# Kernel tuning notes

Hardware: AMD Instinct MI355X
Metric: run time of the kernel (lower is better)

## Reference

```python
import jax, jax.numpy as jnp
import numpy as np

B, DIM, KEY_DIM, NH, AR, RES, KS = 32, 512, 16, 8, 4, 64, 5
D = AR * KEY_DIM          # 64, per-head value dim
C4 = DIM // 4             # 128, q/k channel dim
CHUNK = DIM // NH         # 64, per-head input chunk
SCALE = KEY_DIM ** -0.5


def setup_inputs() -> dict:
    key = jax.random.key(0)
    ks = jax.random.split(key, 8)
    def rn(k, shape, fan):
        return jax.random.normal(k, shape, jnp.float32) * (fan ** -0.5)
    x = jax.random.normal(ks[0], (B, DIM, RES, RES), jnp.float32)
    qk_w = rn(ks[1], (DIM // 2, DIM), DIM)            # fused 1x1 conv+BN weight
    qk_b = jnp.zeros((DIM // 2,), jnp.float32)
    dws_w = rn(ks[2], (C4, 1, KS, KS), KS * KS)        # depthwise conv weight
    dws_b = jnp.zeros((C4,), jnp.float32)
    vs_w = rn(ks[3], (NH, D, CHUNK), CHUNK)            # per-head 1x1 conv weights
    vs_b = jnp.zeros((NH, D), jnp.float32)
    proj_w = rn(ks[4], (DIM, D * NH), D * NH)
    proj_b = jnp.zeros((DIM,), jnp.float32)
    bias_h = jax.random.normal(ks[5], (1, RES), jnp.float32) * 0.02
    bias_w = jax.random.normal(ks[6], (1, RES), jnp.float32) * 0.02
    # offset id for (p1, p2) is exactly |p1 - p2| given enumeration order
    idx = jnp.abs(jnp.arange(RES)[:, None] - jnp.arange(RES)[None, :]).astype(jnp.int32)
    return dict(x=x, qk_w=qk_w, qk_b=qk_b, dws_w=dws_w, dws_b=dws_b,
                vs_w=vs_w, vs_b=vs_b, proj_w=proj_w, proj_b=proj_b,
                bias_h=bias_h, bias_w=bias_w, idx_h=idx, idx_w=idx)


def reference(x, qk_w, qk_b, dws_w, dws_b, vs_w, vs_b, proj_w, proj_b,
              bias_h, bias_w, idx_h, idx_w):
    ab_h = bias_h[0][idx_h]                               # [N, N]
    ab_w = bias_w[0][idx_w]                               # [N, N]
    # qk: fused 1x1 conv + BN -> [B, C/2, H, W]
    feat = jnp.einsum('oc,bchw->bohw', qk_w, x) + qk_b[None, :, None, None]
    q, k = feat[:, :C4], feat[:, C4:]
    # depthwise 5x5 conv on q
    q = jax.lax.conv_general_dilated(
        q, dws_w, (1, 1), 'SAME',
        dimension_numbers=('NCHW', 'OIHW', 'NCHW'),
        feature_group_count=C4) + dws_b[None, :, None, None]
    qr_w = jnp.transpose(q, (0, 2, 3, 1))                 # [B, H, W, C4]
    kr_w = jnp.transpose(k, (0, 2, 3, 1))                 # [B, H, W, C4]
    attn_w = jax.nn.softmax(
        jnp.einsum('bhqc,bhkc->bhqk', qr_w, kr_w) * SCALE + ab_w, axis=-1)
    qr_h = jnp.transpose(qr_w, (0, 2, 1, 3))              # [B, W, H, C4]
    kr_h = jnp.transpose(kr_w, (0, 2, 1, 3))
    attn_h = jax.nn.softmax(
        jnp.einsum('bwqc,bwkc->bwqk', qr_h, kr_h) * SCALE + ab_h, axis=-1)
    # cascaded per-head value chain
    feats_out = []
    feat_i = x[:, :CHUNK]
    for i in range(NH):
        if i > 0:
            feat_i = feat_i + x[:, i * CHUNK:(i + 1) * CHUNK]
        v = jnp.einsum('dc,bchw->bdhw', vs_w[i], feat_i) + vs_b[i][None, :, None, None]
        v = jnp.transpose(v, (0, 2, 3, 1))                # [B, H, W, d]
        v = jnp.einsum('bhqk,bhkd->bhqd', attn_w, v)      # attend along W
        v = jnp.transpose(v, (0, 2, 1, 3))                # [B, W, H, d]
        f = jnp.einsum('bwqk,bwkd->bwqd', attn_h, v)      # attend along H
        feats_out.append(jnp.transpose(f, (0, 3, 2, 1)))  # [B, d, H, W]
    out = jnp.concatenate(feats_out, axis=1)              # [B, d*NH, H, W]
    out = jax.nn.relu(out)
    out = jnp.einsum('oc,bchw->bohw', proj_w, out) + proj_b[None, :, None, None]
    return out
```

## Files before the change

### kernel.cpp

```cpp
#include <hip/hip_runtime.h>

#define PIX 4096
#define SCALE 0.25f

typedef _Float16 f16x8 __attribute__((ext_vector_type(8)));
typedef _Float16 f16x4 __attribute__((ext_vector_type(4)));
typedef float f32x4 __attribute__((ext_vector_type(4)));

__device__ inline void gload_lds16(const _Float16* g, _Float16* l) {
  __builtin_amdgcn_global_load_lds((const __attribute__((address_space(1))) void*)g,
                                   (__attribute__((address_space(3))) void*)l, 16, 0, 0);
}

__global__ __launch_bounds__(256) void k_prep(const float* __restrict__ qk_w,
                                              const float* __restrict__ proj_w,
                                              const float* __restrict__ vs_w,
                                              _Float16* __restrict__ qkw_h,
                                              _Float16* __restrict__ pjw_h,
                                              _Float16* __restrict__ wbig_h) {
  int i = blockIdx.x * 256 + threadIdx.x;
  if (i < 131072) qkw_h[i] = (_Float16)qk_w[i];
  if (i < 262144) {
    pjw_h[i] = (_Float16)proj_w[i];
    int row = i >> 9, col = i & 511;
    int hi = row >> 6, d = row & 63, j = col >> 6, c = col & 63;
    wbig_h[i] = (j <= hi) ? (_Float16)vs_w[hi * 4096 + d * 64 + c] : (_Float16)0;
  }
}

__global__ __launch_bounds__(256) void k_xt(const float* __restrict__ x,
                                            _Float16* __restrict__ xh) {
  __shared__ float tile[64][65];
  int b = blockIdx.z, k0 = blockIdx.y * 64, p0 = blockIdx.x * 64;
  const float* xp = x + ((size_t)b * 512 + k0) * PIX + p0;
  _Float16* out = xh + (size_t)b * PIX * 512;
  int t = threadIdx.x;
  int r = t >> 4, c4 = (t & 15) << 2;
#pragma unroll
  for (int it = 0; it < 4; ++it) {
    float4 v = *(const float4*)&xp[(size_t)(r + it * 16) * PIX + c4];
    tile[r + it * 16][c4 + 0] = v.x; tile[r + it * 16][c4 + 1] = v.y;
    tile[r + it * 16][c4 + 2] = v.z; tile[r + it * 16][c4 + 3] = v.w;
  }
  __syncthreads();
  int pr = t >> 5, kk = (t & 31) << 1;
#pragma unroll
  for (int it = 0; it < 8; ++it) {
    int p = pr + it * 8;
    union { _Float16 h[2]; unsigned int u; } pk;
    pk.h[0] = (_Float16)tile[kk][p]; pk.h[1] = (_Float16)tile[kk + 1][p];
    *(unsigned int*)&out[(size_t)(p0 + p) * 512 + k0 + kk] = pk.u;
  }
}

template<int MODE>
__global__ __launch_bounds__(512, 2)
void k_mg8(const _Float16* __restrict__ A,
           const _Float16* __restrict__ B,
           const float* __restrict__ bias,
           const _Float16* __restrict__ attn,
           float* C, _Float16* H, _Float16* H2, int nwg_m) {
  constexpr int MROWS = (MODE == 1) ? 128 : 256;
  constexpr int AH = MROWS * 32;
  constexpr int SLOT = AH + 8192;
  constexpr int MI = MROWS / 32;
  constexpr int DEPTH = (MODE == 2) ? 3 : 1;
  constexpr int NSLOT = (MODE == 2) ? 4 : 2;
  constexpr int LDSH = (MODE == 2) ? NSLOT * SLOT : 32768;
  __shared__ __align__(16) _Float16 lds[LDSH];
  int nwg = gridDim.x;
  int id = blockIdx.x;
  int qq = nwg >> 3;
  id = (id & 7) * qq + (id >> 3);
  int mb = id % nwg_m;
  int rest = id / nwg_m;
  int pb = rest & 15;
  int b  = rest >> 4;
  int m0 = mb * MROWS, p0 = pb * 256;
  int t = threadIdx.x, wid = t >> 6, lane = t & 63;
  int wm = wid >> 2, wn = wid & 3;
  int lr = lane & 15, q4 = lane >> 4;
  const _Float16* Ab = A + (size_t)m0 * 512;
  const _Float16* Bp = B + (size_t)b * 2097152 + (size_t)p0 * 512;

  int nt = (MODE == 1) ? ((m0 + 128) >> 6) : 8;
  int nsub = nt * 2;

  auto STAGE = [&](int g) {
    int slot = g % NSLOT;
    _Float16* dA = lds + slot * SLOT;
    _Float16* dB = dA + AH;
    size_t ks = (size_t)g * 32;
    if constexpr (MODE == 1) {
      int L = wid * 64 + lane;
      int row = L >> 2, sl = L & 3;
      int c = sl ^ ((row >> 1) & 3);
      gload_lds16(Ab + (size_t)row * 512 + ks + c * 8, dA + (size_t)(wid * 64) * 8);
    } else {
#pragma unroll
      for (int is = 0; is < 2; ++is) {
        int L = is * 512 + wid * 64 + lane;
        int row = L >> 2, sl = L & 3;
        int c = sl ^ ((row >> 1) & 3);
        gload_lds16(Ab + (size_t)row * 512 + ks + c * 8, dA + (size_t)(is * 512 + wid * 64) * 8);
      }
    }
#pragma unroll
    for (int is = 0; is < 2; ++is) {
      int L = is * 512 + wid * 64 + lane;
      int row = L >> 2, sl = L & 3;
      int c = sl ^ ((row >> 1) & 3);
      gload_lds16(Bp + (size_t)row * 512 + ks + c * 8, dB + (size_t)(is * 512 + wid * 64) * 8);
    }
  };

  f32x4 acc[MI][4] = {};
  if constexpr (DEPTH == 3) { STAGE(0); STAGE(1); STAGE(2); }
  else STAGE(0);
  for (int n = 0; n < nsub; ++n) {
    if (n + DEPTH < nsub) STAGE(n + DEPTH);
    int r = nsub - 1 - n; if (r > DEPTH) r = DEPTH;
    if constexpr (MODE == 1) {
      if (r >= 1) asm volatile("s_waitcnt vmcnt(3)" ::: "memory");
      else        asm volatile("s_waitcnt vmcnt(0)" ::: "memory");
    } else if constexpr (MODE == 0) {
      if (r >= 1) asm volatile("s_waitcnt vmcnt(4)" ::: "memory");
      else        asm volatile("s_waitcnt vmcnt(0)" ::: "memory");
    } else {
      if (r == 3)      asm volatile("s_waitcnt vmcnt(12)" ::: "memory");
      else if (r == 2) asm volatile("s_waitcnt vmcnt(8)" ::: "memory");
      else if (r == 1) asm volatile("s_waitcnt vmcnt(4)" ::: "memory");
      else             asm volatile("s_waitcnt vmcnt(0)" ::: "memory");
    }
    __builtin_amdgcn_s_barrier();
    const _Float16* A_s = lds + (n % NSLOT) * SLOT;
    const _Float16* B_s = A_s + AH;
    f16x8 af[MI], bf[4];
#pragma unroll
    for (int mi = 0; mi < MI; ++mi) {
      int row = wm * (MROWS / 2) + mi * 16 + lr;
      af[mi] = *(const f16x8*)&A_s[row * 32 + ((q4 ^ ((row >> 1) & 3)) << 3)];
    }
#pragma unroll
    for (int ni = 0; ni < 4; ++ni) {
      int row = wn * 64 + ni * 16 + lr;
      bf[ni] = *(const f16x8*)&B_s[row * 32 + ((q4 ^ ((row >> 1) & 3)) << 3)];
    }
    __builtin_amdgcn_s_setprio(1);
#pragma unroll
    for (int mi = 0; mi < MI; ++mi)
#pragma unroll
      for (int ni = 0; ni < 4; ++ni)
        acc[mi][ni] = __builtin_amdgcn_mfma_f32_16x16x32_f16(af[mi], bf[ni], acc[mi][ni], 0, 0, 0);
    __builtin_amdgcn_s_setprio(0);
    __builtin_amdgcn_s_barrier();
  }

  if (MODE == 0) {
#pragma unroll
    for (int mi = 0; mi < MI; ++mi)
#pragma unroll
      for (int rr = 0; rr < 4; ++rr) {
        int m = m0 + wm * 128 + mi * 16 + q4 * 4 + rr;
        float bi = bias[m];
        float* crow = C + ((size_t)b * 512 + m) * PIX + p0 + wn * 64;
#pragma unroll
        for (int ni = 0; ni < 4; ++ni)
          crow[ni * 16 + lr] = acc[mi][ni][rr] + bi;
      }
  }

  if (MODE == 1) {
    _Float16* Cs = lds + wid * 4096;
#pragma unroll
    for (int mi = 0; mi < 4; ++mi)
#pragma unroll
      for (int ni = 0; ni < 4; ++ni)
#pragma unroll
        for (int rr = 0; rr < 4; ++rr) {
          int row = mi * 16 + q4 * 4 + rr;
          int col = ni * 16 + lr;
          Cs[row * 64 + ((((col >> 3) ^ (row & 7)) << 3) | (col & 7))] =
              (_Float16)(acc[mi][ni][rr] + bias[m0 + wm * 64 + row]);
        }
    int s = pb * 4 + wn;
    const _Float16* Ab2 = attn + ((size_t)b * 64 + s) * 4096;
    f16x8 bfr[4][2];
#pragma unroll
    for (int ni = 0; ni < 4; ++ni)
#pragma unroll
      for (int kk = 0; kk < 2; ++kk)
        bfr[ni][kk] = *(const f16x8*)&Ab2[(ni * 16 + lr) * 64 + q4 * 8 + kk * 32];
    f32x4 acc2[4][4] = {};
#pragma unroll
    for (int mi2 = 0; mi2 < 4; ++mi2)
#pragma unroll
      for (int kk = 0; kk < 2; ++kk) {
        int row = mi2 * 16 + lr;
        f16x8 afr = *(const f16x8*)&Cs[row * 64 + (((q4 + kk * 4) ^ (row & 7)) << 3)];
#pragma unroll
        for (int ni2 = 0; ni2 < 4; ++ni2)
          acc2[mi2][ni2] = __builtin_amdgcn_mfma_f32_16x16x32_f16(afr, bfr[ni2][kk], acc2[mi2][ni2], 0, 0, 0);
      }
#pragma unroll
    for (int mi2 = 0; mi2 < 4; ++mi2)
#pragma unroll
      for (int rr = 0; rr < 4; ++rr) {
        int m = m0 + wm * 64 + mi2 * 16 + q4 * 4 + rr;
        _Float16* crow = H + ((size_t)b * 512 + m) * PIX + p0 + wn * 64;
#pragma unroll
        for (int ni2 = 0; ni2 < 4; ++ni2)
          crow[ni2 * 16 + lr] = (_Float16)acc2[mi2][ni2][rr];
      }
  }

  if (MODE == 2) {
    if (wm == 0) {
#pragma unroll
      for (int mi = 0; mi < MI; ++mi)
#pragma unroll
        for (int rr = 0; rr < 4; ++rr) {
          int m = mi * 16 + q4 * 4 + rr;
          float bi = bias[m];
          _Float16* crow = H2 + ((size_t)b * 128 + m) * PIX + p0 + wn * 64;
#pragma unroll
          for (int ni = 0; ni < 4; ++ni)
            crow[ni * 16 + lr] = (_Float16)(acc[mi][ni][rr] + bi);
        }
    } else {
      _Float16* Ls = lds + (size_t)(wid - 4) * 16384;
#pragma unroll
      for (int mi = 0; mi < MI; ++mi)
#pragma unroll
        for (int ni = 0; ni < 4; ++ni)
#pragma unroll
          for (int rr = 0; rr < 4; ++rr) {
            int ch = mi * 16 + q4 * 4 + rr;
            Ls[(ni * 16 + lr) * 136 + ch] = (_Float16)(acc[mi][ni][rr] + bias[128 + ch]);
          }
      _Float16* khb = H + ((size_t)b * PIX + p0 + wn * 64) * 128;
#pragma unroll
      for (int it = 0; it < 16; ++it) {
        int chk = it * 64 + lane;
        int prow = chk >> 4, cc = (chk & 15) << 3;
        *(f16x8*)&khb[(size_t)prow * 128 + cc] = *(const f16x8*)&Ls[prow * 136 + cc];
      }
    }
  }
}

__global__ __launch_bounds__(256) void k_dwconv(const _Float16* __restrict__ feat,
                                                const float* __restrict__ w,
                                                const float* __restrict__ bias,
                                                _Float16* __restrict__ qc) {
  __shared__ float tile[68][68];
  int c = blockIdx.x, b = blockIdx.y;
  const _Float16* in = feat + ((size_t)b * 128 + c) * PIX;
  float wreg[25];
#pragma unroll
  for (int i = 0; i < 25; ++i) wreg[i] = w[c * 25 + i];
  float bi = bias[c];
  int t = threadIdx.x;
  for (int idx = t; idx < 68 * 68; idx += 256) {
    int y = idx / 68, xx = idx - y * 68;
    int h = y - 2, ww = xx - 2;
    float v = 0.f;
    if (h >= 0 && h < 64 && ww >= 0 && ww < 64) v = (float)in[h * 64 + ww];
    tile[y][xx] = v;
  }
  __syncthreads();
  _Float16* out = qc + ((size_t)b * 128 + c) * PIX;
  int tx = (t & 15) << 2, ty = (t >> 4) << 2;
#pragma unroll
  for (int i = 0; i < 4; ++i) {
    f16x4 o;
#pragma unroll
    for (int j = 0; j < 4; ++j) {
      float s = bi;
#pragma unroll
      for (int dy = 0; dy < 5; ++dy)
#pragma unroll
        for (int dx = 0; dx < 5; ++dx)
          s += wreg[dy * 5 + dx] * tile[ty + i + dy][tx + j + dx];
      o[j] = (_Float16)s;
    }
    *(f16x4*)&out[(ty + i) * 64 + tx] = o;
  }
}

__global__ __launch_bounds__(256) void k_qkt16(const _Float16* __restrict__ in,
                                               _Float16* __restrict__ out) {
  __shared__ __align__(16) _Float16 Ts[64 * 136];
  int p0 = blockIdx.x * 64, b = blockIdx.y;
  const _Float16* ip = in + (size_t)b * 128 * PIX;
  int t = threadIdx.x;
#pragma unroll
  for (int it = 0; it < 4; ++it) {
    int i4 = it * 256 + t;
    int c = i4 >> 3, pc = (i4 & 7) << 3;
    f16x8 v = *(const f16x8*)&ip[(size_t)c * PIX + p0 + pc];
#pragma unroll
    for (int j = 0; j < 8; ++j) Ts[(pc + j) * 136 + c] = v[j];
  }
  __syncthreads();
  _Float16* op = out + (size_t)b * (PIX * 128) + (size_t)p0 * 128;
#pragma unroll
  for (int it = 0; it < 4; ++it) {
    int ch = it * 256 + t;
    int p = ch >> 4, cc = (ch & 15) << 3;
    *(f16x8*)&op[p * 128 + cc] = *(const f16x8*)&Ts[p * 136 + cc];
  }
}

__global__ __launch_bounds__(256) void k_mattn(const _Float16* __restrict__ qh,
                                               const _Float16* __restrict__ kh,
                                               const float* __restrict__ bias_w,
                                               const float* __restrict__ bias_h,
                                               _Float16* __restrict__ attnW,
                                               _Float16* __restrict__ attnH) {
  __shared__ __align__(16) _Float16 Qs[64 * 136];
  __shared__ __align__(16) _Float16 Ks[64 * 136];
  __shared__ float bl[64];
  int j = blockIdx.x, b = blockIdx.y, which = blockIdx.z;
  const float* bias = which ? bias_h : bias_w;
  _Float16* attn = which ? attnH : attnW;
  int t = threadIdx.x;
  if (t < 64) bl[t] = bias[t];
  const _Float16* qb = qh + (size_t)b * (PIX * 128);
  const _Float16* kb = kh + (size_t)b * (PIX * 128);
#pragma unroll
  for (int it = 0; it < 4; ++it) {
    int idx = it * 256 + t;
    int r = idx >> 4, cc = (idx & 15) << 3;
    size_t p = which ? (size_t)(j + 64 * r) : (size_t)(j * 64 + r);
    *(f16x8*)&Qs[r * 136 + cc] = *(const f16x8*)&qb[p * 128 + cc];
    *(f16x8*)&Ks[r * 136 + cc] = *(const f16x8*)&kb[p * 128 + cc];
  }
  __syncthreads();
  int wave = t >> 6, lane = t & 63;
  int lr = lane & 15, q4 = lane >> 4;
  f16x8 af[4];
#pragma unroll
  for (int kk = 0; kk < 4; ++kk)
    af[kk] = *(const f16x8*)&Qs[(wave * 16 + lr) * 136 + q4 * 8 + kk * 32];
  f32x4 acc[4] = {};
#pragma unroll
  for (int ni = 0; ni < 4; ++ni)
#pragma unroll
    for (int kk = 0; kk < 4; ++kk) {
      f16x8 bf = *(const f16x8*)&Ks[(ni * 16 + lr) * 136 + q4 * 8 + kk * 32];
      acc[ni] = __builtin_amdgcn_mfma_f32_16x16x32_f16(af[kk], bf, acc[ni], 0, 0, 0);
    }
  float ev[4][4], sm[4];
#pragma unroll
  for (int r = 0; r < 4; ++r) {
    int qrow = wave * 16 + q4 * 4 + r;
    float m = -1e30f;
#pragma unroll
    for (int ni = 0; ni < 4; ++ni) {
      int k = ni * 16 + lr;
      ev[ni][r] = acc[ni][r] * SCALE + bl[abs(qrow - k)];
      m = fmaxf(m, ev[ni][r]);
    }
    m = fmaxf(m, __shfl_xor(m, 1)); m = fmaxf(m, __shfl_xor(m, 2));
    m = fmaxf(m, __shfl_xor(m, 4)); m = fmaxf(m, __shfl_xor(m, 8));
    float s = 0.f;
#pragma unroll
    for (int ni = 0; ni < 4; ++ni) { ev[ni][r] = __expf(ev[ni][r] - m); s += ev[ni][r]; }
    s += __shfl_xor(s, 1); s += __shfl_xor(s, 2);
    s += __shfl_xor(s, 4); s += __shfl_xor(s, 8);
    sm[r] = 1.f / s;
  }
  _Float16* ab = attn + (((size_t)b * 64 + j) * 64) * 64;
#pragma unroll
  for (int r = 0; r < 4; ++r) {
    int qrow = wave * 16 + q4 * 4 + r;
#pragma unroll
    for (int ni = 0; ni < 4; ++ni)
      ab[qrow * 64 + ni * 16 + lr] = (_Float16)(ev[ni][r] * sm[r]);
  }
}

__global__ __launch_bounds__(256) void k_hmix(const _Float16* __restrict__ tT,
                                              const _Float16* __restrict__ attnH,
                                              _Float16* __restrict__ ght) {
  __shared__ __align__(16) _Float16 Ts[128 * 64];
  __shared__ __align__(16) _Float16 Ls[64 * 136];
  int id = blockIdx.x;
  int ct = id & 3, w = (id >> 2) & 63, b = id >> 8;
  int t = threadIdx.x, wid = t >> 6, lane = t & 63;
  int lr = lane & 15, q4 = lane >> 4;
  const _Float16* Tb = tT + ((size_t)b * 512 + ct * 128) * PIX + w * 64;
#pragma unroll
  for (int it = 0; it < 4; ++it) {
    int idx = it * 256 + t;
    int row = idx >> 3, c = idx & 7;
    int sc = c ^ (row & 7);
    gload_lds16(Tb + (size_t)row * PIX + sc * 8, &Ts[(it * 256 + wid * 64) * 8]);
  }
  const _Float16* Ab = attnH + ((size_t)b * 64 + w) * 4096;
  f16x8 bfr[4][2];
#pragma unroll
  for (int ni = 0; ni < 4; ++ni)
#pragma unroll
    for (int kk = 0; kk < 2; ++kk)
      bfr[ni][kk] = *(const f16x8*)&Ab[(ni * 16 + lr) * 64 + q4 * 8 + kk * 32];
  __syncthreads();
  f32x4 acc[2][4] = {};
#pragma unroll
  for (int mi = 0; mi < 2; ++mi) {
    int rr = wid * 32 + mi * 16 + lr;
#pragma unroll
    for (int kk = 0; kk < 2; ++kk) {
      f16x8 af = *(const f16x8*)&Ts[rr * 64 + (((q4 + 4 * kk) ^ (rr & 7)) << 3)];
#pragma unroll
      for (int ni = 0; ni < 4; ++ni)
        acc[mi][ni] = __builtin_amdgcn_mfma_f32_16x16x32_f16(af, bfr[ni][kk], acc[mi][ni], 0, 0, 0);
    }
  }
#pragma unroll
  for (int mi = 0; mi < 2; ++mi)
#pragma unroll
    for (int ni = 0; ni < 4; ++ni)
#pragma unroll
      for (int rr = 0; rr < 4; ++rr) {
        float v = acc[mi][ni][rr];
        Ls[(ni * 16 + lr) * 136 + wid * 32 + mi * 16 + q4 * 4 + rr] =
            (_Float16)(v > 0.f ? v : 0.f);
      }
  __syncthreads();
  _Float16* gb = ght + (size_t)b * PIX * 512 + ct * 128;
#pragma unroll
  for (int it = 0; it < 4; ++it) {
    int idx = it * 256 + t;
    int hp = idx >> 4, cc = (idx & 15) << 3;
    *(f16x8*)&gb[((size_t)hp * 64 + w) * 512 + cc] = *(const f16x8*)&Ls[hp * 136 + cc];
  }
}

__global__ __launch_bounds__(256) void k_t16(const _Float16* __restrict__ in,
                                             _Float16* __restrict__ out) {
  __shared__ _Float16 tile[64][65];
  int img = blockIdx.x;
  const _Float16* ip = in + (size_t)img * PIX;
  _Float16* op = out + (size_t)img * PIX;
  int t = threadIdx.x;
  int col = t & 63, r0 = t >> 6;
  for (int it = 0; it < 16; ++it) {
    int r = r0 + it * 4;
    tile[r][col] = ip[r * 64 + col];
  }
  __syncthreads();
  for (int it = 0; it < 16; ++it) {
    int r = r0 + it * 4;
    op[r * 64 + col] = tile[col][r];
  }
}

extern "C" void kernel_launch(void* const* d_in, const int* in_sizes, int n_in,
                              void* d_out, int out_size, void* d_ws, size_t ws_size,
                              hipStream_t stream) {
  const float* x      = (const float*)d_in[0];
  const float* qk_w   = (const float*)d_in[1];
  const float* qk_b   = (const float*)d_in[2];
  const float* dws_w  = (const float*)d_in[3];
  const float* dws_b  = (const float*)d_in[4];
  const float* vs_w   = (const float*)d_in[5];
  const float* vs_b   = (const float*)d_in[6];
  const float* proj_w = (const float*)d_in[7];
  const float* proj_b = (const float*)d_in[8];
  const float* bias_h = (const float*)d_in[9];
  const float* bias_w = (const float*)d_in[10];

  float* ws = (float*)d_ws;
  float* dout = (float*)d_out;

  _Float16* xh    = (_Float16*)ws;
  _Float16* ght   = xh;
  _Float16* tT    = (_Float16*)(ws + 33554432);
  _Float16* attnW = (_Float16*)(ws + 67108864);
  _Float16* attnH = (_Float16*)(ws + 71303168);
  _Float16* qkw_h  = (_Float16*)(ws + 75497472);
  _Float16* wbig_h = (_Float16*)(ws + 75563008);
  _Float16* pjw_h  = (_Float16*)(ws + 75694080);

  _Float16* feat_h = (_Float16*)dout;
  _Float16* qc_h   = (_Float16*)(dout + 8388608);
  _Float16* qh     = (_Float16*)(dout + 16777216);
  _Float16* kh     = (_Float16*)(dout + 25165824);
  _Float16* Vh     = (_Float16*)(dout + 33554432);

  k_prep<<<1024, 256, 0, stream>>>(qk_w, proj_w, vs_w, qkw_h, pjw_h, wbig_h);
  k_xt<<<dim3(64, 8, 32), 256, 0, stream>>>(x, xh);
  k_mg8<2><<<512, 512, 0, stream>>>(qkw_h, xh, qk_b, nullptr, nullptr, kh, feat_h, 1);
  k_dwconv<<<dim3(128, 32), 256, 0, stream>>>(feat_h, dws_w, dws_b, qc_h);
  k_qkt16<<<dim3(64, 32), 256, 0, stream>>>(qc_h, qh);
  k_mattn<<<dim3(64, 32, 2), 256, 0, stream>>>(qh, kh, bias_w, bias_h, attnW, attnH);
  k_mg8<1><<<2048, 512, 0, stream>>>(wbig_h, xh, vs_b, attnW, nullptr, Vh, nullptr, 4);
  k_t16<<<32 * 512, 256, 0, stream>>>(Vh, tT);
  k_hmix<<<8192, 256, 0, stream>>>(tT, attnH, ght);
  k_mg8<0><<<1024, 512, 0, stream>>>(pjw_h, ght, proj_b, nullptr, dout, nullptr, nullptr, 2);
}
```

Baseline: 568.1 us.

## Fuse transpose into H-axis attention mix kernel, dropping intermediate buffer

```diff
diff --git a/kernel.cpp b/kernel.cpp
--- a/kernel.cpp
+++ b/kernel.cpp
@@ -381,79 +381,61 @@
   }
 }
 
-__global__ __launch_bounds__(256) void k_hmix(const _Float16* __restrict__ tT,
-                                              const _Float16* __restrict__ attnH,
-                                              _Float16* __restrict__ ght) {
-  __shared__ __align__(16) _Float16 Ts[128 * 64];
-  __shared__ __align__(16) _Float16 Ls[64 * 136];
-  int id = blockIdx.x;
-  int ct = id & 3, w = (id >> 2) & 63, b = id >> 8;
-  int t = threadIdx.x, wid = t >> 6, lane = t & 63;
+__global__ __launch_bounds__(512, 2) void k_thmix(const _Float16* __restrict__ t,
+                                                  const _Float16* __restrict__ attnH,
+                                                  _Float16* __restrict__ ght) {
+  __shared__ __align__(16) _Float16 T[16 * 32 * 72];
+  int nwg = gridDim.x;
+  int p = blockIdx.x;
+  int l = (p & 7) * (nwg >> 3) + (p >> 3);
+  int wlo = l & 3, cht = (l >> 2) & 15, b = l >> 6;
+  int w0 = wlo * 16;
+  int tid = threadIdx.x, wid = tid >> 6, lane = tid & 63;
   int lr = lane & 15, q4 = lane >> 4;
-  const _Float16* Tb = tT + ((size_t)b * 512 + ct * 128) * PIX + w * 64;
-#pragma unroll
-  for (int it = 0; it < 4; ++it) {
-    int idx = it * 256 + t;
-    int row = idx >> 3, c = idx & 7;
-    int sc = c ^ (row & 7);
-    gload_lds16(Tb + (size_t)row * PIX + sc * 8, &Ts[(it * 256 + wid * 64) * 8]);
-  }
-  const _Float16* Ab = attnH + ((size_t)b * 64 + w) * 4096;
-  f16x8 bfr[4][2];
-#pragma unroll
-  for (int ni = 0; ni < 4; ++ni)
-#pragma unroll
-    for (int kk = 0; kk < 2; ++kk)
-      bfr[ni][kk] = *(const f16x8*)&Ab[(ni * 16 + lr) * 64 + q4 * 8 + kk * 32];
+  const _Float16* tb = t + ((size_t)b * 512 + cht * 32) * PIX + w0;
+#pragma unroll
+  for (int it = 0; it < 8; ++it) {
+    int chunk = it * 512 + tid;
+    int c = chunk >> 7, rem = chunk & 127;
+    int h = rem >> 1, wh = rem & 1;
+    f16x8 v = *(const f16x8*)&tb[(size_t)c * PIX + h * 64 + wh * 8];
+#pragma unroll
+    for (int j = 0; j < 8; ++j)
+      T[((wh * 8 + j) * 32 + c) * 72 + h] = v[j];
+  }
   __syncthreads();
-  f32x4 acc[2][4] = {};
-#pragma unroll
-  for (int mi = 0; mi < 2; ++mi) {
-    int rr = wid * 32 + mi * 16 + lr;
-#pragma unroll
-    for (int kk = 0; kk < 2; ++kk) {
-      f16x8 af = *(const f16x8*)&Ts[rr * 64 + (((q4 + 4 * kk) ^ (rr & 7)) << 3)];
-#pragma unroll
-      for (int ni = 0; ni < 4; ++ni)
-        acc[mi][ni] = __builtin_amdgcn_mfma_f32_16x16x32_f16(af, bfr[ni][kk], acc[mi][ni], 0, 0, 0);
-    }
-  }
-#pragma unroll
-  for (int mi = 0; mi < 2; ++mi)
+  _Float16* gb = ght + (size_t)b * PIX * 512 + cht * 32;
+  for (int wi = 0; wi < 2; ++wi) {
+    int w = wid * 2 + wi;
+    const _Float16* Ab = attnH + ((size_t)b * 64 + w0 + w) * 4096;
+    f16x8 bfr[4][2];
 #pragma unroll
     for (int ni = 0; ni < 4; ++ni)
 #pragma unroll
-      for (int rr = 0; rr < 4; ++rr) {
-        float v = acc[mi][ni][rr];
-        Ls[(ni * 16 + lr) * 136 + wid * 32 + mi * 16 + q4 * 4 + rr] =
-            (_Float16)(v > 0.f ? v : 0.f);
-      }
-  __syncthreads();
-  _Float16* gb = ght + (size_t)b * PIX * 512 + ct * 128;
-#pragma unroll
-  for (int it = 0; it < 4; ++it) {
-    int idx = it * 256 + t;
-    int hp = idx >> 4, cc = (idx & 15) << 3;
-    *(f16x8*)&gb[((size_t)hp * 64 + w) * 512 + cc] = *(const f16x8*)&Ls[hp * 136 + cc];
-  }
-}
-
-__global__ __launch_bounds__(256) void k_t16(const _Float16* __restrict__ in,
-                                             _Float16* __restrict__ out) {
-  __shared__ _Float16 tile[64][65];
-  int img = blockIdx.x;
-  const _Float16* ip = in + (size_t)img * PIX;
-  _Float16* op = out + (size_t)img * PIX;
-  int t = threadIdx.x;
-  int col = t & 63, r0 = t >> 6;
-  for (int it = 0; it < 16; ++it) {
-    int r = r0 + it * 4;
-    tile[r][col] = ip[r * 64 + col];
-  }
-  __syncthreads();
-  for (int it = 0; it < 16; ++it) {
-    int r = r0 + it * 4;
-    op[r * 64 + col] = tile[col][r];
+      for (int kk = 0; kk < 2; ++kk)
+        bfr[ni][kk] = *(const f16x8*)&Ab[(ni * 16 + lr) * 64 + q4 * 8 + kk * 32];
+    f32x4 acc[2][4] = {};
+#pragma unroll
+    for (int mf = 0; mf < 2; ++mf)
+#pragma unroll
+      for (int kk = 0; kk < 2; ++kk) {
+        f16x8 af = *(const f16x8*)&T[(w * 32 + mf * 16 + lr) * 72 + q4 * 8 + kk * 32];
+#pragma unroll
+        for (int ni = 0; ni < 4; ++ni)
+          acc[mf][ni] = __builtin_amdgcn_mfma_f32_16x16x32_f16(af, bfr[ni][kk], acc[mf][ni], 0, 0, 0);
+      }
+#pragma unroll
+    for (int mf = 0; mf < 2; ++mf)
+#pragma unroll
+      for (int ni = 0; ni < 4; ++ni) {
+        f16x4 o;
+#pragma unroll
+        for (int r = 0; r < 4; ++r) {
+          float v = acc[mf][ni][r];
+          o[r] = (_Float16)(v > 0.f ? v : 0.f);
+        }
+        *(f16x4*)&gb[((size_t)(ni * 16 + lr) * 64 + w0 + w) * 512 + mf * 16 + q4 * 4] = o;
+      }
   }
 }
 
@@ -477,7 +459,6 @@
 
   _Float16* xh    = (_Float16*)ws;
   _Float16* ght   = xh;
-  _Float16* tT    = (_Float16*)(ws + 33554432);
   _Float16* attnW = (_Float16*)(ws + 67108864);
   _Float16* attnH = (_Float16*)(ws + 71303168);
   _Float16* qkw_h  = (_Float16*)(ws + 75497472);
@@ -497,7 +478,6 @@
   k_qkt16<<<dim3(64, 32), 256, 0, stream>>>(qc_h, qh);
   k_mattn<<<dim3(64, 32, 2), 256, 0, stream>>>(qh, kh, bias_w, bias_h, attnW, attnH);
   k_mg8<1><<<2048, 512, 0, stream>>>(wbig_h, xh, vs_b, attnW, nullptr, Vh, nullptr, 4);
-  k_t16<<<32 * 512, 256, 0, stream>>>(Vh, tT);
-  k_hmix<<<8192, 256, 0, stream>>>(tT, attnH, ght);
+  k_thmix<<<2048, 512, 0, stream>>>(Vh, attnH, ght);
   k_mg8<0><<<1024, 512, 0, stream>>>(pjw_h, ght, proj_b, nullptr, dout, nullptr, nullptr, 2);
 }
```

Measured after the change: 550.5 us, median of 2. 1.03x faster.
